# Optimization experiments

Measured on AMD Instinct MI355X. Metric: run time of the kernel, lower is better.

## Reference

```python
import jax, jax.numpy as jnp
import numpy as np

L = 3          # n_layers
B = 512        # batch
H = 1024       # d_model == d_enopt (last-layer hidden is fed back as input)
T = 8          # num_targets
TAU = 96       # decode steps
BETA = 2.0     # softplus beta


def setup_inputs() -> dict:
    key = jax.random.key(0)
    ks = jax.random.split(key, 10)
    s = 0.02
    return {
        "hidden": jax.random.normal(ks[0], (L, B, H), jnp.float32),
        "cell":   jax.random.normal(ks[1], (L, B, H), jnp.float32),
        # stacked per-layer LSTM weights (input size == H for all layers)
        "W_ih": jax.random.normal(ks[2], (L, 4 * H, H), jnp.float32) * s,
        "W_hh": jax.random.normal(ks[3], (L, 4 * H, H), jnp.float32) * s,
        "b_ih": jax.random.normal(ks[4], (L, 4 * H), jnp.float32) * s,
        "b_hh": jax.random.normal(ks[5], (L, 4 * H), jnp.float32) * s,
        "W1": jax.random.normal(ks[6], (T, H), jnp.float32) * s,
        "b1": jax.random.normal(ks[7], (T,), jnp.float32) * s,
        "W2": jax.random.normal(ks[8], (T, H), jnp.float32) * s,
        "b2": jax.random.normal(ks[9], (T,), jnp.float32) * s,
    }


def _lstm_step(h, c, W_ih, W_hh, b_ih, b_hh):
    x = h[-1]  # [B, H]
    new_h, new_c = [], []
    for l in range(L):
        gates = x @ W_ih[l].T + b_ih[l] + h[l] @ W_hh[l].T + b_hh[l]  # [B, 4H]
        i, f, g, o = jnp.split(gates, 4, axis=-1)  # PyTorch gate order i,f,g,o
        i, f, o = jax.nn.sigmoid(i), jax.nn.sigmoid(f), jax.nn.sigmoid(o)
        g = jnp.tanh(g)
        c_l = f * c[l] + i * g
        h_l = o * jnp.tanh(c_l)
        new_h.append(h_l)
        new_c.append(c_l)
        x = h_l  # input to next layer (dropout inactive at inference)
    return jnp.stack(new_h), jnp.stack(new_c), x


def reference(hidden, cell, W_ih, W_hh, b_ih, b_hh, W1, b1, W2, b2):
    def step(carry, _):
        h, c = carry
        h, c, y = _lstm_step(h, c, W_ih, W_hh, b_ih, b_hh)
        return (h, c), y

    (_, _), ys = jax.lax.scan(step, (hidden, cell), None, length=TAU)  # ys: [TAU, B, H]
    out = jnp.transpose(ys, (1, 0, 2))  # [B, TAU, H] (batch_first concat over time)
    mu = out @ W1.T + b1
    sigma = jax.nn.softplus(BETA * (out @ W2.T + b2)) / BETA
    return mu, sigma
```

## Files before the change

### kernel.cpp

```cpp
#include <hip/hip_runtime.h>
#include <stdint.h>


typedef __attribute__((ext_vector_type(8))) short short8;
typedef __attribute__((ext_vector_type(8))) __bf16 bf16x8_t;
typedef __attribute__((ext_vector_type(4))) float f32x4;
typedef __attribute__((ext_vector_type(4))) unsigned short u16x4;

static __device__ __forceinline__ unsigned short f2bf(float f) {
  unsigned int u = __float_as_uint(f);
  u += 0x7FFFu + ((u >> 16) & 1u);
  return (unsigned short)(u >> 16);
}

static __device__ __forceinline__ float sigm(float x) {
  return 1.0f / (1.0f + __expf(-x));
}
static __device__ __forceinline__ float tanh_f(float x) {
  float xc = fminf(fmaxf(x, -15.f), 15.f);
  float e = __expf(2.0f * xc);
  return 1.0f - 2.0f / (e + 1.0f);
}

static __device__ __forceinline__ void gload_lds16_sc0(const void* g, void* l) {
  __builtin_amdgcn_global_load_lds(
      (const __attribute__((address_space(1))) unsigned int*)g,
      (__attribute__((address_space(3))) unsigned int*)l, 16, 0, 1);
}

static __device__ __forceinline__ f32x4 ld4_sc0(const float* p) {
  f32x4 r;
  asm volatile("global_load_dwordx4 %0, %1, off sc0"
               : "=v"(r) : "v"(p) : "memory");
  return r;
}
#define VMCNT0 asm volatile("s_waitcnt vmcnt(0)" ::: "memory")

static __device__ __forceinline__ f32x4 mfma16(short8 a, short8 b, f32x4 c) {
  return __builtin_amdgcn_mfma_f32_16x16x32_bf16((bf16x8_t)a, (bf16x8_t)b, c, 0, 0, 0);
}

__global__ __launch_bounds__(256, 1) void persist_kernel(
    const unsigned short* __restrict__ WihA,
    const unsigned short* __restrict__ WhhA,
    unsigned short* __restrict__ hB,
    float* __restrict__ cS,
    float* __restrict__ gB,
    const float* __restrict__ biasA,
    float* __restrict__ macc,
    const float* __restrict__ W1, const float* __restrict__ W2,
    unsigned* __restrict__ bar) {
  __shared__ __align__(16) char ldsA[3][32768];

  unsigned xcc;
  asm volatile("s_getreg_b32 %0, hwreg(HW_REG_XCC_ID)" : "=s"(xcc));
  xcc &= 7u;

  int* shmeta = (int*)ldsA[2];
  if (threadIdx.x == 0) {
    unsigned t = __hip_atomic_fetch_add(bar + 256 + xcc * 32, 1u,
                                        __ATOMIC_RELAXED,
                                        __HIP_MEMORY_SCOPE_AGENT);
    shmeta[0] = (int)t;
  }
  __syncthreads();
  const int ticket = shmeta[0];
  const int mt = (int)xcc;
  const int role = ticket & 1;
  const int hcg = ticket >> 1;
  const int tile = hcg * 8 + mt;
  const int m0 = mt * 64;
  const int hc0 = hcg * 64;
  unsigned* mybar = bar + xcc * 32;

  const int tid = threadIdx.x;
  const int w = tid >> 6;
  const int lane = tid & 63;
  const int quad = lane >> 4;
  const int l16 = lane & 15;
  const int rbase = tid >> 5;
  const int spos = tid & 31;
  const int wvbase = w * 1024;
  const int rx0 = l16, rx1 = 16 + l16;

#define STAGE(kc_, buf_)                                                      \
  {                                                                           \
    _Pragma("unroll") for (int j = 0; j < 8; ++j) {                           \
      int r_ = j * 8 + rbase;                                                 \
      int c_ = spos ^ (r_ & 31);                                              \
      gload_lds16_sc0(Ap + (size_t)(m0 + r_) * 1024 + (kc_)*256 + c_ * 8,     \
                      &ldsA[buf_][j * 4096 + wvbase]);                        \
    }                                                                         \
  }

#pragma unroll 1
  for (int p = 0; p < 289; ++p) {
    const int l = (p == 0) ? 2 : (p - 1) % 3;
    const int st = (p == 0) ? 0 : (p - 1) / 3;
    const int lh = (l + 1) % 3;
    const int do_x = (p != 0);
    const int do_h = (p != 288);
    const int do_proj = (p != 0) && (l == 2);
    const int active = role ? do_h : do_x;

    if (active) {
      const unsigned short* Wp;
      const unsigned short* Ap;
      if (role) {
        Wp = WhhA + (size_t)lh * 4194304;
        Ap = hB + (size_t)lh * 524288;
      } else {
        Wp = WihA + (size_t)l * 4194304;
        Ap = hB + (size_t)((l == 0) ? 2 : (l - 1)) * 524288;
      }

      const unsigned short* brow[4];
#pragma unroll
      for (int g = 0; g < 4; ++g)
        brow[g] = Wp + (size_t)(g * 1024 + hc0 + w * 16 + l16) * 1024 + quad * 8;

      STAGE(0, 0);
      short8 bfr[4][4];
#pragma unroll
      for (int d = 0; d < 4; ++d)
#pragma unroll
        for (int g = 0; g < 4; ++g) bfr[d][g] = *(const short8*)(brow[g] + d * 32);

      f32x4 acc[4][4];
      if (role == 0) {
        const float* gb_rd = gB + (size_t)l * 2097152;
#pragma unroll
        for (int mb = 0; mb < 4; ++mb)
#pragma unroll
          for (int g = 0; g < 4; ++g)
            acc[mb][g] = ld4_sc0(
                gb_rd + ((size_t)(tile * 4 + w) * 16 + g * 4 + mb) * 256 + lane * 4);
        VMCNT0;
        __builtin_amdgcn_sched_barrier(0);
      } else {
        f32x4 z4 = {0.f, 0.f, 0.f, 0.f};
#pragma unroll
        for (int mb = 0; mb < 4; ++mb)
#pragma unroll
          for (int g = 0; g < 4; ++g) acc[mb][g] = z4;
      }
      __syncthreads();

#pragma unroll
      for (int kc = 0; kc < 4; ++kc) {
        if (kc < 3) STAGE(kc + 1, (kc + 1) & 1);
        const char* base = ldsA[kc & 1];
        short8 afr[2][4];
#pragma unroll
        for (int mb = 0; mb < 4; ++mb) {
          int rxm = (mb & 1) ? rx1 : rx0;
          afr[0][mb] =
              *(const short8*)(base + (mb * 16 + l16) * 512 + ((quad ^ rxm) << 4));
        }
#pragma unroll
        for (int ks = 0; ks < 8; ++ks) {
          const int kg = kc * 8 + ks;
          short8 a0 = afr[ks & 1][0], a1 = afr[ks & 1][1];
          short8 a2 = afr[ks & 1][2], a3 = afr[ks & 1][3];
          short8 b0 = bfr[kg & 3][0], b1 = bfr[kg & 3][1];
          short8 b2 = bfr[kg & 3][2], b3 = bfr[kg & 3][3];
          if (ks < 7) {
#pragma unroll
            for (int mb = 0; mb < 4; ++mb) {
              int rxm = (mb & 1) ? rx1 : rx0;
              afr[(ks + 1) & 1][mb] =
                  *(const short8*)(base + (mb * 16 + l16) * 512 +
                                   ((((ks + 1) * 4 + quad) ^ rxm) << 4));
            }
          }
          if (kg + 4 < 32) {
#pragma unroll
            for (int g = 0; g < 4; ++g)
              bfr[kg & 3][g] = *(const short8*)(brow[g] + (kg + 4) * 32);
          }
          acc[0][0] = mfma16(a0, b0, acc[0][0]);
          acc[1][0] = mfma16(a1, b0, acc[1][0]);
          acc[2][0] = mfma16(a2, b0, acc[2][0]);
          acc[3][0] = mfma16(a3, b0, acc[3][0]);
          acc[0][1] = mfma16(a0, b1, acc[0][1]);
          acc[1][1] = mfma16(a1, b1, acc[1][1]);
          acc[2][1] = mfma16(a2, b1, acc[2][1]);
          acc[3][1] = mfma16(a3, b1, acc[3][1]);
          acc[0][2] = mfma16(a0, b2, acc[0][2]);
          acc[1][2] = mfma16(a1, b2, acc[1][2]);
          acc[2][2] = mfma16(a2, b2, acc[2][2]);
          acc[3][2] = mfma16(a3, b2, acc[3][2]);
          acc[0][3] = mfma16(a0, b3, acc[0][3]);
          acc[1][3] = mfma16(a1, b3, acc[1][3]);
          acc[2][3] = mfma16(a2, b3, acc[2][3]);
          acc[3][3] = mfma16(a3, b3, acc[3][3]);
        }
        if (kc < 3) __syncthreads();
      }

      if (role == 1) {
        float* gb_wr = gB + (size_t)lh * 2097152;
#pragma unroll
        for (int mb = 0; mb < 4; ++mb)
#pragma unroll
          for (int g = 0; g < 4; ++g)
            *(f32x4*)(gb_wr + ((size_t)(tile * 4 + w) * 16 + g * 4 + mb) * 256 +
                      lane * 4) = acc[mb][g];
      } else {
        float* c_l = cS + (size_t)l * 524288;
        unsigned short* h_out = hB + (size_t)l * 524288;
        const float* bias_l = biasA + l * 4096;
        const int colh = hc0 + w * 16 + l16;
        float bs0 = bias_l[colh];
        float bs1 = bias_l[1024 + colh];
        float bs2 = bias_l[2048 + colh];
        float bs3 = bias_l[3072 + colh];
        float hv[16];
#pragma unroll
        for (int mb = 0; mb < 4; ++mb) {
#pragma unroll
          for (int rr = 0; rr < 4; ++rr) {
            int row = m0 + mb * 16 + quad * 4 + rr;
            float gi = acc[mb][0][rr] + bs0;
            float gf = acc[mb][1][rr] + bs1;
            float gg = acc[mb][2][rr] + bs2;
            float go = acc[mb][3][rr] + bs3;
            float* cp = c_l + (size_t)row * 1024 + colh;
            float cn = sigm(gf) * (*cp) + sigm(gi) * tanh_f(gg);
            *cp = cn;
            float h = sigm(go) * tanh_f(cn);
            hv[mb * 4 + rr] = h;
            h_out[(size_t)row * 1024 + colh] = f2bf(h);
          }
        }

        if (do_proj) {
          float* hbuf = (float*)ldsA[0];
          float* projred = (float*)ldsA[1];
#pragma unroll
          for (int mb = 0; mb < 4; ++mb)
#pragma unroll
            for (int rr = 0; rr < 4; ++rr)
              hbuf[(mb * 16 + quad * 4 + rr) * 65 + w * 16 + l16] = hv[mb * 4 + rr];
          __syncthreads();

          const int m = tid & 63;
          const int grp = tid >> 6;
          float pm[8], ps[8];
          float hj[16];
#pragma unroll
          for (int j = 0; j < 16; ++j) hj[j] = hbuf[m * 65 + grp * 16 + j];
#pragma unroll
          for (int tt = 0; tt < 8; ++tt) {
            const f32x4* w1p = (const f32x4*)(W1 + tt * 1024 + hc0 + grp * 16);
            const f32x4* w2p = (const f32x4*)(W2 + tt * 1024 + hc0 + grp * 16);
            float s1 = 0.f, s2 = 0.f;
#pragma unroll
            for (int v = 0; v < 4; ++v) {
              f32x4 wa = w1p[v], wb = w2p[v];
#pragma unroll
              for (int j = 0; j < 4; ++j) {
                s1 += hj[v * 4 + j] * wa[j];
                s2 += hj[v * 4 + j] * wb[j];
              }
            }
            pm[tt] = s1;
            ps[tt] = s2;
          }
#pragma unroll
          for (int tt = 0; tt < 8; ++tt) {
            projred[(grp * 64 + m) * 17 + tt] = pm[tt];
            projred[(grp * 64 + m) * 17 + 8 + tt] = ps[tt];
          }
          __syncthreads();
#pragma unroll
          for (int q = 0; q < 4; ++q) {
            int s = grp * 4 + q;
            float v = projred[m * 17 + s] + projred[(64 + m) * 17 + s] +
                      projred[(128 + m) * 17 + s] + projred[(192 + m) * 17 + s];
            atomicAdd(&macc[((size_t)(m0 + m) * 96 + st) * 16 + s], v);
          }
        }
      }
    }

    if (p < 288) {
      VMCNT0;
      __syncthreads();
      if (tid == 0) {
        __hip_atomic_fetch_add(mybar, 1u, __ATOMIC_RELAXED,
                               __HIP_MEMORY_SCOPE_AGENT);
        const unsigned tgt = 32u * (unsigned)(p + 1);
        while (__hip_atomic_load(mybar, __ATOMIC_RELAXED,
                                 __HIP_MEMORY_SCOPE_AGENT) < tgt)
          __builtin_amdgcn_s_sleep(2);
      }
      asm volatile("" ::: "memory");
      __syncthreads();
    }
  }
#undef STAGE
}

__global__ void conv_w(const f32x4* __restrict__ wi, const f32x4* __restrict__ wh,
                       u16x4* __restrict__ wib, u16x4* __restrict__ whb) {
  int i = blockIdx.x * 256 + threadIdx.x;
  f32x4 a = wi[i], b = wh[i];
  u16x4 pa, pb;
#pragma unroll
  for (int j = 0; j < 4; ++j) {
    pa[j] = f2bf(a[j]);
    pb[j] = f2bf(b[j]);
  }
  wib[i] = pa;
  whb[i] = pb;
}

__global__ void init_state(const f32x4* __restrict__ hid, const f32x4* __restrict__ cel,
                           const f32x4* __restrict__ bih, const f32x4* __restrict__ bhh,
                           u16x4* __restrict__ hb, f32x4* __restrict__ cs,
                           f32x4* __restrict__ bias) {
  int i = blockIdx.x * 256 + threadIdx.x;
  f32x4 h = hid[i];
  u16x4 p;
#pragma unroll
  for (int j = 0; j < 4; ++j) p[j] = f2bf(h[j]);
  hb[i] = p;
  cs[i] = cel[i];
  if (i < 3072) bias[i] = bih[i] + bhh[i];
}

__global__ void finalize_k(const float* __restrict__ macc, const float* __restrict__ b1,
                           const float* __restrict__ b2, float* __restrict__ out) {
  int idx = blockIdx.x * 256 + threadIdx.x;
  int t = idx & 7;
  int bt = idx >> 3;
  float mu = macc[bt * 16 + t] + b1[t];
  float z2 = 2.0f * (macc[bt * 16 + 8 + t] + b2[t]);
  float sp = fmaxf(z2, 0.f) + log1pf(__expf(-fabsf(z2)));
  out[idx] = mu;
  out[393216 + idx] = 0.5f * sp;
}

extern "C" void kernel_launch(void* const* d_in, const int* in_sizes, int n_in,
                              void* d_out, int out_size, void* d_ws, size_t ws_size,
                              hipStream_t stream) {
  (void)in_sizes; (void)n_in; (void)out_size; (void)ws_size;
  const float* hidden = (const float*)d_in[0];
  const float* cell = (const float*)d_in[1];
  const float* Wih = (const float*)d_in[2];
  const float* Whh = (const float*)d_in[3];
  const float* bih = (const float*)d_in[4];
  const float* bhh = (const float*)d_in[5];
  const float* W1 = (const float*)d_in[6];
  const float* b1 = (const float*)d_in[7];
  const float* W2 = (const float*)d_in[8];
  const float* b2 = (const float*)d_in[9];
  float* out = (float*)d_out;

  char* ws = (char*)d_ws;
  unsigned short* Wih_b = (unsigned short*)(ws);
  unsigned short* Whh_b = (unsigned short*)(ws + 25165824);
  unsigned short* h_b = (unsigned short*)(ws + 50331648);
  float* c_s = (float*)(ws + 53477376);
  float* gbuf = (float*)(ws + 59768832);
  float* bias = (float*)(ws + 84934656);
  float* macc = (float*)(ws + 84983808);
  unsigned* bar = (unsigned*)(ws + 88129536);

  hipMemsetAsync(macc, 0, 3145728, stream);
  hipMemsetAsync(bar, 0, 2048, stream);
  conv_w<<<12288, 256, 0, stream>>>((const f32x4*)Wih, (const f32x4*)Whh,
                                    (u16x4*)Wih_b, (u16x4*)Whh_b);
  init_state<<<1536, 256, 0, stream>>>((const f32x4*)hidden, (const f32x4*)cell,
                                       (const f32x4*)bih, (const f32x4*)bhh,
                                       (u16x4*)h_b, (f32x4*)c_s, (f32x4*)bias);

  persist_kernel<<<256, 256, 0, stream>>>(Wih_b, Whh_b, h_b, c_s, gbuf, bias,
                                          macc, W1, W2, bar);

  finalize_k<<<1536, 256, 0, stream>>>(macc, b1, b2, out);
}
```

Before: 9.304 ms.

## Halve per-block hidden-column tile and launch twice as many persistent blocks

Each block now covers 32 hidden columns instead of 64, with the four waves arranged as 2 column groups by 2 row halves, so each wave holds a 2x4 accumulator grid instead of 4x4. The grid doubles to 512 blocks with launch bounds allowing 2 blocks per CU, and LDS is trimmed to two buffers so two blocks fit. The per-XCC barrier target doubles to match. This spreads the weight streaming over more blocks and adds occupancy to hide latency, at the cost of each block re-staging the same A tile and more barrier participants per step.

```diff
diff --git a/kernel.cpp b/kernel.cpp
--- a/kernel.cpp
+++ b/kernel.cpp
@@ -40,7 +40,7 @@
   return __builtin_amdgcn_mfma_f32_16x16x32_bf16((bf16x8_t)a, (bf16x8_t)b, c, 0, 0, 0);
 }
 
-__global__ __launch_bounds__(256, 1) void persist_kernel(
+__global__ __launch_bounds__(256, 2) void persist_kernel(
     const unsigned short* __restrict__ WihA,
     const unsigned short* __restrict__ WhhA,
     unsigned short* __restrict__ hB,
@@ -50,13 +50,13 @@
     float* __restrict__ macc,
     const float* __restrict__ W1, const float* __restrict__ W2,
     unsigned* __restrict__ bar) {
-  __shared__ __align__(16) char ldsA[3][32768];
+  __shared__ __align__(16) char ldsA[2][32768];
+  __shared__ int shmeta[4];
 
   unsigned xcc;
   asm volatile("s_getreg_b32 %0, hwreg(HW_REG_XCC_ID)" : "=s"(xcc));
   xcc &= 7u;
 
-  int* shmeta = (int*)ldsA[2];
   if (threadIdx.x == 0) {
     unsigned t = __hip_atomic_fetch_add(bar + 256 + xcc * 32, 1u,
                                         __ATOMIC_RELAXED,
@@ -67,14 +67,16 @@
   const int ticket = shmeta[0];
   const int mt = (int)xcc;
   const int role = ticket & 1;
-  const int hcg = ticket >> 1;
-  const int tile = hcg * 8 + mt;
+  const int hcg5 = ticket >> 1;
+  const int tile = hcg5 * 8 + mt;
   const int m0 = mt * 64;
-  const int hc0 = hcg * 64;
+  const int hc0 = hcg5 * 32;
   unsigned* mybar = bar + xcc * 32;
 
   const int tid = threadIdx.x;
   const int w = tid >> 6;
+  const int cg = w & 1;
+  const int rh = w >> 1;
   const int lane = tid & 63;
   const int quad = lane >> 4;
   const int l16 = lane & 15;
@@ -117,7 +119,8 @@
       const unsigned short* brow[4];
 #pragma unroll
       for (int g = 0; g < 4; ++g)
-        brow[g] = Wp + (size_t)(g * 1024 + hc0 + w * 16 + l16) * 1024 + quad * 8;
+        brow[g] =
+            Wp + (size_t)(g * 1024 + hc0 + cg * 16 + l16) * 1024 + quad * 8;
 
       STAGE(0, 0);
       short8 bfr[4][4];
@@ -126,21 +129,23 @@
 #pragma unroll
         for (int g = 0; g < 4; ++g) bfr[d][g] = *(const short8*)(brow[g] + d * 32);
 
-      f32x4 acc[4][4];
+      f32x4 acc[2][4];
       if (role == 0) {
         const float* gb_rd = gB + (size_t)l * 2097152;
 #pragma unroll
-        for (int mb = 0; mb < 4; ++mb)
+        for (int mb = 0; mb < 2; ++mb)
 #pragma unroll
           for (int g = 0; g < 4; ++g)
             acc[mb][g] = ld4_sc0(
-                gb_rd + ((size_t)(tile * 4 + w) * 16 + g * 4 + mb) * 256 + lane * 4);
+                gb_rd +
+                ((size_t)((tile * 2 + cg) * 16) + g * 4 + rh * 2 + mb) * 256 +
+                lane * 4);
         VMCNT0;
         __builtin_amdgcn_sched_barrier(0);
       } else {
         f32x4 z4 = {0.f, 0.f, 0.f, 0.f};
 #pragma unroll
-        for (int mb = 0; mb < 4; ++mb)
+        for (int mb = 0; mb < 2; ++mb)
 #pragma unroll
           for (int g = 0; g < 4; ++g) acc[mb][g] = z4;
       }
@@ -150,26 +155,25 @@
       for (int kc = 0; kc < 4; ++kc) {
         if (kc < 3) STAGE(kc + 1, (kc + 1) & 1);
         const char* base = ldsA[kc & 1];
-        short8 afr[2][4];
-#pragma unroll
-        for (int mb = 0; mb < 4; ++mb) {
+        short8 afr[2][2];
+#pragma unroll
+        for (int mb = 0; mb < 2; ++mb) {
           int rxm = (mb & 1) ? rx1 : rx0;
-          afr[0][mb] =
-              *(const short8*)(base + (mb * 16 + l16) * 512 + ((quad ^ rxm) << 4));
+          afr[0][mb] = *(const short8*)(base + (rh * 32 + mb * 16 + l16) * 512 +
+                                        ((quad ^ rxm) << 4));
         }
 #pragma unroll
         for (int ks = 0; ks < 8; ++ks) {
           const int kg = kc * 8 + ks;
           short8 a0 = afr[ks & 1][0], a1 = afr[ks & 1][1];
-          short8 a2 = afr[ks & 1][2], a3 = afr[ks & 1][3];
           short8 b0 = bfr[kg & 3][0], b1 = bfr[kg & 3][1];
           short8 b2 = bfr[kg & 3][2], b3 = bfr[kg & 3][3];
           if (ks < 7) {
 #pragma unroll
-            for (int mb = 0; mb < 4; ++mb) {
+            for (int mb = 0; mb < 2; ++mb) {
               int rxm = (mb & 1) ? rx1 : rx0;
               afr[(ks + 1) & 1][mb] =
-                  *(const short8*)(base + (mb * 16 + l16) * 512 +
+                  *(const short8*)(base + (rh * 32 + mb * 16 + l16) * 512 +
                                    ((((ks + 1) * 4 + quad) ^ rxm) << 4));
             }
           }
@@ -180,20 +184,12 @@
           }
           acc[0][0] = mfma16(a0, b0, acc[0][0]);
           acc[1][0] = mfma16(a1, b0, acc[1][0]);
-          acc[2][0] = mfma16(a2, b0, acc[2][0]);
-          acc[3][0] = mfma16(a3, b0, acc[3][0]);
           acc[0][1] = mfma16(a0, b1, acc[0][1]);
           acc[1][1] = mfma16(a1, b1, acc[1][1]);
-          acc[2][1] = mfma16(a2, b1, acc[2][1]);
-          acc[3][1] = mfma16(a3, b1, acc[3][1]);
           acc[0][2] = mfma16(a0, b2, acc[0][2]);
           acc[1][2] = mfma16(a1, b2, acc[1][2]);
-          acc[2][2] = mfma16(a2, b2, acc[2][2]);
-          acc[3][2] = mfma16(a3, b2, acc[3][2]);
           acc[0][3] = mfma16(a0, b3, acc[0][3]);
           acc[1][3] = mfma16(a1, b3, acc[1][3]);
-          acc[2][3] = mfma16(a2, b3, acc[2][3]);
-          acc[3][3] = mfma16(a3, b3, acc[3][3]);
         }
         if (kc < 3) __syncthreads();
       }
@@ -201,26 +197,28 @@
       if (role == 1) {
         float* gb_wr = gB + (size_t)lh * 2097152;
 #pragma unroll
-        for (int mb = 0; mb < 4; ++mb)
+        for (int mb = 0; mb < 2; ++mb)
 #pragma unroll
           for (int g = 0; g < 4; ++g)
-            *(f32x4*)(gb_wr + ((size_t)(tile * 4 + w) * 16 + g * 4 + mb) * 256 +
+            *(f32x4*)(gb_wr +
+                      ((size_t)((tile * 2 + cg) * 16) + g * 4 + rh * 2 + mb) *
+                          256 +
                       lane * 4) = acc[mb][g];
       } else {
         float* c_l = cS + (size_t)l * 524288;
         unsigned short* h_out = hB + (size_t)l * 524288;
         const float* bias_l = biasA + l * 4096;
-        const int colh = hc0 + w * 16 + l16;
+        const int colh = hc0 + cg * 16 + l16;
         float bs0 = bias_l[colh];
         float bs1 = bias_l[1024 + colh];
         float bs2 = bias_l[2048 + colh];
         float bs3 = bias_l[3072 + colh];
-        float hv[16];
-#pragma unroll
-        for (int mb = 0; mb < 4; ++mb) {
+        float hv[8];
+#pragma unroll
+        for (int mb = 0; mb < 2; ++mb) {
 #pragma unroll
           for (int rr = 0; rr < 4; ++rr) {
-            int row = m0 + mb * 16 + quad * 4 + rr;
+            int row = m0 + rh * 32 + mb * 16 + quad * 4 + rr;
             float gi = acc[mb][0][rr] + bs0;
             float gf = acc[mb][1][rr] + bs1;
             float gg = acc[mb][2][rr] + bs2;
@@ -238,25 +236,26 @@
           float* hbuf = (float*)ldsA[0];
           float* projred = (float*)ldsA[1];
 #pragma unroll
-          for (int mb = 0; mb < 4; ++mb)
+          for (int mb = 0; mb < 2; ++mb)
 #pragma unroll
             for (int rr = 0; rr < 4; ++rr)
-              hbuf[(mb * 16 + quad * 4 + rr) * 65 + w * 16 + l16] = hv[mb * 4 + rr];
+              hbuf[(rh * 32 + mb * 16 + quad * 4 + rr) * 33 + cg * 16 + l16] =
+                  hv[mb * 4 + rr];
           __syncthreads();
 
           const int m = tid & 63;
           const int grp = tid >> 6;
           float pm[8], ps[8];
-          float hj[16];
-#pragma unroll
-          for (int j = 0; j < 16; ++j) hj[j] = hbuf[m * 65 + grp * 16 + j];
+          float hj[8];
+#pragma unroll
+          for (int j = 0; j < 8; ++j) hj[j] = hbuf[m * 33 + grp * 8 + j];
 #pragma unroll
           for (int tt = 0; tt < 8; ++tt) {
-            const f32x4* w1p = (const f32x4*)(W1 + tt * 1024 + hc0 + grp * 16);
-            const f32x4* w2p = (const f32x4*)(W2 + tt * 1024 + hc0 + grp * 16);
+            const f32x4* w1p = (const f32x4*)(W1 + tt * 1024 + hc0 + grp * 8);
+            const f32x4* w2p = (const f32x4*)(W2 + tt * 1024 + hc0 + grp * 8);
             float s1 = 0.f, s2 = 0.f;
 #pragma unroll
-            for (int v = 0; v < 4; ++v) {
+            for (int v = 0; v < 2; ++v) {
               f32x4 wa = w1p[v], wb = w2p[v];
 #pragma unroll
               for (int j = 0; j < 4; ++j) {
@@ -290,7 +289,7 @@
       if (tid == 0) {
         __hip_atomic_fetch_add(mybar, 1u, __ATOMIC_RELAXED,
                                __HIP_MEMORY_SCOPE_AGENT);
-        const unsigned tgt = 32u * (unsigned)(p + 1);
+        const unsigned tgt = 64u * (unsigned)(p + 1);
         while (__hip_atomic_load(mybar, __ATOMIC_RELAXED,
                                  __HIP_MEMORY_SCOPE_AGENT) < tgt)
           __builtin_amdgcn_s_sleep(2);
@@ -376,7 +375,7 @@
                                        (const f32x4*)bih, (const f32x4*)bhh,
                                        (u16x4*)h_b, (f32x4*)c_s, (f32x4*)bias);
 
-  persist_kernel<<<256, 256, 0, stream>>>(Wih_b, Whh_b, h_b, c_s, gbuf, bias,
+  persist_kernel<<<512, 256, 0, stream>>>(Wih_b, Whh_b, h_b, c_s, gbuf, bias,
                                           macc, W1, W2, bar);
 
   finalize_k<<<1536, 256, 0, stream>>>(macc, b1, b2, out);
```

After: 13.41 ms. 1.44x slower.
